# Optimization experiments

Hardware: AMD Instinct MI355X
Metric: run time of the kernel (lower is better)

The kernel has to match this reference:

```python
import jax, jax.numpy as jnp
import numpy as np

K_NEIGHBORS = 9
BN_EPS = 1e-5


def _bn(x, g, b, m, v):
    # inference-mode BatchNorm over channel (last) axis
    return (x - m) * (g / jnp.sqrt(v + BN_EPS)) + b


def _sincos_1d(dim, pos):
    half = dim // 2
    omega = 1.0 / (10000.0 ** (jnp.arange(half, dtype=jnp.float32) / half))
    ang = pos[:, None] * omega[None, :]
    return jnp.concatenate([jnp.sin(ang), jnp.cos(ang)], axis=1)


def _pos_embed_2d(dim, H, W):
    # standard 2D sin-cos positional embedding, (N, dim)
    yy, xx = jnp.meshgrid(jnp.arange(H, dtype=jnp.float32), jnp.arange(W, dtype=jnp.float32), indexing='ij')
    emb_h = _sincos_1d(dim // 2, yy.reshape(-1))
    emb_w = _sincos_1d(dim // 2, xx.reshape(-1))
    return jnp.concatenate([emb_h, emb_w], axis=1)


def setup_inputs() -> dict:
    key = jax.random.key(0)
    ks = jax.random.split(key, 8)
    B, C, H, W = 8, 192, 56, 56
    C2 = 2 * C
    Cg = C2 // 4  # per-group channels for grouped 1x1 conv
    x = jax.random.normal(ks[0], (B, C, H, W), jnp.float32)
    inp = {
        'x': x,
        'fc1_w': jax.random.normal(ks[1], (C, C), jnp.float32) * 0.05,
        'fc1_b': jnp.zeros((C,), jnp.float32),
        'bn1_g': jnp.ones((C,), jnp.float32),
        'bn1_b': jnp.zeros((C,), jnp.float32),
        'bn1_m': jax.random.normal(ks[2], (C,), jnp.float32) * 0.1,
        'bn1_v': jax.random.uniform(ks[3], (C,), jnp.float32, 0.5, 1.5),
        'gc_w': jax.random.normal(ks[4], (4, Cg, Cg), jnp.float32) * 0.05,  # groups=4, (g, out_pg, in_pg)
        'gc_b': jnp.zeros((C2,), jnp.float32),
        'bng_g': jnp.ones((C2,), jnp.float32),
        'bng_b': jnp.zeros((C2,), jnp.float32),
        'bng_m': jax.random.normal(ks[5], (C2,), jnp.float32) * 0.1,
        'bng_v': jax.random.uniform(ks[6], (C2,), jnp.float32, 0.5, 1.5),
        'fc2_w': jax.random.normal(ks[7], (C, C2), jnp.float32) * 0.05,
        'fc2_b': jnp.zeros((C,), jnp.float32),
        'bn2_g': jnp.ones((C,), jnp.float32),
        'bn2_b': jnp.zeros((C,), jnp.float32),
        'bn2_m': jnp.zeros((C,), jnp.float32),
        'bn2_v': jnp.ones((C,), jnp.float32),
    }
    return inp


def reference(x, fc1_w, fc1_b, bn1_g, bn1_b, bn1_m, bn1_v,
              gc_w, gc_b, bng_g, bng_b, bng_m, bng_v,
              fc2_w, fc2_b, bn2_g, bn2_b, bn2_m, bn2_v):
    B, C, H, W = x.shape
    N = H * W
    shortcut = x
    # fc1: 1x1 conv + BN, working in (B, N, C) layout
    h = x.reshape(B, C, N).transpose(0, 2, 1)
    h = jnp.einsum('bnc,dc->bnd', h, fc1_w) + fc1_b
    h = _bn(h, bn1_g, bn1_b, bn1_m, bn1_v)
    # relative position bias (ViG-style: -2*pe@pe.T/dim)
    pe = _pos_embed_2d(C, H, W)                      # (N, C)
    rel = (-2.0 / C) * (pe @ pe.T)                   # (N, N)
    # dense dilated kNN graph on L2-normalized features
    xn = h / jnp.maximum(jnp.linalg.norm(h, axis=-1, keepdims=True), 1e-12)
    sq = jnp.sum(xn * xn, axis=-1, keepdims=True)    # (B, N, 1)
    dist = sq - 2.0 * jnp.einsum('bnc,bmc->bnm', xn, xn) + sq.transpose(0, 2, 1)
    dist = dist + rel[None]                          # (B, N, N)
    _, nn_idx = jax.lax.top_k(-dist, K_NEIGHBORS)    # (B, N, K), dilation=1
    # MRConv2d: max-relative aggregation
    x_j = h[jnp.arange(B)[:, None, None], nn_idx]    # (B, N, K, C) gather
    d = jnp.max(x_j - h[:, :, None, :], axis=2)      # (B, N, C)
    g = jnp.concatenate([h, d], axis=-1)             # (B, N, 2C)
    # grouped 1x1 conv (groups=4) + BN + GELU
    C2 = 2 * C
    Cg = C2 // 4
    gg = g.reshape(B, N, 4, Cg)
    y = jnp.einsum('bngc,gdc->bngd', gg, gc_w).reshape(B, N, C2) + gc_b
    y = jax.nn.gelu(_bn(y, bng_g, bng_b, bng_m, bng_v), approximate=False)
    # fc2: 1x1 conv + BN, residual
    o = jnp.einsum('bnc,dc->bnd', y, fc2_w) + fc2_b
    o = _bn(o, bn2_g, bn2_b, bn2_m, bn2_v)
    out = o.transpose(0, 2, 1).reshape(B, C, H, W) + shortcut
    return out
```

## Files before the change

kernel.cpp:

```cpp
#include <hip/hip_runtime.h>
#include <math.h>

#define BATCH 8
#define CH    192
#define WW    56
#define NPTS  3136
#define C2    384
#define CG    96
#define MT    32
#define MSPLIT 4
#define LK    12
#define NCAND (MSPLIT*LK)
#define NREF  16
#define MQ    (NPTS/MSPLIT)

typedef float f32x4 __attribute__((ext_vector_type(4)));
typedef short bf16x8 __attribute__((ext_vector_type(8)));

__device__ __forceinline__ float gelu_exact(float v) {
  return 0.5f * v * (1.0f + erff(v * 0.7071067811865475f));
}
__device__ __forceinline__ unsigned short f2bf(float f) {
  unsigned int u = __float_as_uint(f);
  u = u + 0x7fffu + ((u >> 16) & 1u);
  return (unsigned short)(u >> 16);
}
__device__ __forceinline__ float bf2f(unsigned short h) {
  return __uint_as_float(((unsigned int)h) << 16);
}
__device__ __forceinline__ void gl_lds16(const void* g, void* lds) {
  __builtin_amdgcn_global_load_lds(
      (const __attribute__((address_space(1))) unsigned int*)g,
      (__attribute__((address_space(3))) unsigned int*)lds, 16, 0, 0);
}
__device__ __forceinline__ unsigned fmono(float f) {
  unsigned u = __float_as_uint(f);
  return u ^ ((unsigned)((int)u >> 31) | 0x80000000u);
}
__device__ __forceinline__ unsigned umin32(unsigned a, unsigned b) { return a < b ? a : b; }
__device__ __forceinline__ unsigned umax32(unsigned a, unsigned b) { return a < b ? b : a; }

__global__ void prep_kernel(
    const float* __restrict__ fc1_w, const float* __restrict__ fc1_b,
    const float* __restrict__ bn1_g, const float* __restrict__ bn1_b,
    const float* __restrict__ bn1_m, const float* __restrict__ bn1_v,
    const float* __restrict__ gc_w,  const float* __restrict__ gc_b,
    const float* __restrict__ bng_g, const float* __restrict__ bng_b,
    const float* __restrict__ bng_m, const float* __restrict__ bng_v,
    const float* __restrict__ fc2_w, const float* __restrict__ fc2_b,
    const float* __restrict__ bn2_g, const float* __restrict__ bn2_b,
    const float* __restrict__ bn2_m, const float* __restrict__ bn2_v,
    float* __restrict__ w1, float* __restrict__ b1,
    unsigned short* __restrict__ wgh, unsigned short* __restrict__ wgl,
    float* __restrict__ bg,
    unsigned short* __restrict__ w2h, unsigned short* __restrict__ w2l,
    float* __restrict__ b2, float* __restrict__ ftab)
{
  int i = blockIdx.x * 256 + threadIdx.x;
  if (i < 36864) {
    int d = i / CH;
    float s = bn1_g[d] / sqrtf(bn1_v[d] + 1e-5f);
    w1[i] = fc1_w[i] * s;
  } else if (i < 37056) {
    int d = i - 36864;
    float s = bn1_g[d] / sqrtf(bn1_v[d] + 1e-5f);
    b1[d] = (fc1_b[d] - bn1_m[d]) * s + bn1_b[d];
  } else if (i < 73920) {
    int j = i - 37056;
    int o = j / CG;
    float s = bng_g[o] / sqrtf(bng_v[o] + 1e-5f);
    float v = gc_w[j] * s;
    unsigned short hi = f2bf(v);
    wgh[j] = hi;
    wgl[j] = f2bf(v - bf2f(hi));
  } else if (i < 74304) {
    int o = i - 73920;
    float s = bng_g[o] / sqrtf(bng_v[o] + 1e-5f);
    bg[o] = (gc_b[o] - bng_m[o]) * s + bng_b[o];
  } else if (i < 148032) {
    int j = i - 74304;
    int d = j / C2;
    float s = bn2_g[d] / sqrtf(bn2_v[d] + 1e-5f);
    float v = fc2_w[j] * s;
    unsigned short hi = f2bf(v);
    w2h[j] = hi;
    w2l[j] = f2bf(v - bf2f(hi));
  } else if (i < 148224) {
    int d = i - 148032;
    float s = bn2_g[d] / sqrtf(bn2_v[d] + 1e-5f);
    b2[d] = (fc2_b[d] - bn2_m[d]) * s + bn2_b[d];
  } else if (i < 148280) {
    int delta = i - 148224;
    float s = 0.f;
    for (int t = 0; t < 48; ++t) {
      float omega = powf(10000.f, -(float)t / 48.f);
      s += cosf((float)delta * omega);
    }
    ftab[delta] = s * (-2.0f / (float)CH);
  }
}

__global__ __launch_bounds__(256) void fc1_kernel(
    const float* __restrict__ x, const float* __restrict__ w1,
    const float* __restrict__ b1, float* __restrict__ h)
{
  __shared__ float As[64*68];
  __shared__ float Bs[64*68];
  const int tid = threadIdx.x;
  const int ntile = blockIdx.x, dt = blockIdx.y, b = blockIdx.z;
  const int n0 = ntile * 64, d0 = dt * 64;
  const int ty = tid >> 4, tx = tid & 15;
  const float* xb = x + (size_t)b * CH * NPTS;
  float acc[4][4] = {};
  for (int k0 = 0; k0 < CH; k0 += 64) {
    if (k0) __syncthreads();
#pragma unroll
    for (int p = 0; p < 16; ++p) {
      int e = p * 256 + tid;
      int kk = e >> 6, r = e & 63;
      As[r*68 + kk] = xb[(size_t)(k0 + kk) * NPTS + n0 + r];
    }
#pragma unroll
    for (int p = 0; p < 4; ++p) {
      int e = p * 256 + tid;
      int dd = e >> 4, k4 = (e & 15) << 2;
      *(float4*)&Bs[dd*68 + k4] = *(const float4*)&w1[(size_t)(d0 + dd) * CH + k0 + k4];
    }
    __syncthreads();
#pragma unroll
    for (int kq = 0; kq < 16; ++kq) {
      float4 av[4], bv[4];
#pragma unroll
      for (int i = 0; i < 4; ++i) av[i] = *(const float4*)&As[(ty*4+i)*68 + kq*4];
#pragma unroll
      for (int j = 0; j < 4; ++j) bv[j] = *(const float4*)&Bs[(tx*4+j)*68 + kq*4];
#pragma unroll
      for (int i = 0; i < 4; ++i)
#pragma unroll
        for (int j = 0; j < 4; ++j)
          acc[i][j] += av[i].x*bv[j].x + av[i].y*bv[j].y + av[i].z*bv[j].z + av[i].w*bv[j].w;
    }
  }
#pragma unroll
  for (int i = 0; i < 4; ++i) {
    int n = n0 + ty*4 + i;
    float4 v;
    v.x = acc[i][0] + b1[d0 + tx*4 + 0];
    v.y = acc[i][1] + b1[d0 + tx*4 + 1];
    v.z = acc[i][2] + b1[d0 + tx*4 + 2];
    v.w = acc[i][3] + b1[d0 + tx*4 + 3];
    *(float4*)&h[((size_t)b * NPTS + n) * CH + d0 + tx*4] = v;
  }
}

__global__ __launch_bounds__(256) void norm_kernel(
    const float* __restrict__ h, float* __restrict__ xnf,
    unsigned short* __restrict__ xhi, unsigned short* __restrict__ xlo,
    float* __restrict__ sqv)
{
  const int lane = threadIdx.x & 63;
  const int row = blockIdx.x * 4 + (threadIdx.x >> 6);
  const float* hr = h + (size_t)row * CH;
  float v0 = hr[lane], v1 = hr[lane + 64], v2 = hr[lane + 128];
  float s = v0*v0 + v1*v1 + v2*v2;
#pragma unroll
  for (int o = 32; o > 0; o >>= 1) s += __shfl_xor(s, o);
  float inv = 1.0f / fmaxf(sqrtf(s), 1e-12f);
  float x0 = v0 * inv, x1 = v1 * inv, x2 = v2 * inv;
  size_t base = (size_t)row * CH;
  xnf[base + lane      ] = x0;
  xnf[base + lane + 64 ] = x1;
  xnf[base + lane + 128] = x2;
  unsigned short h0 = f2bf(x0), h1 = f2bf(x1), h2 = f2bf(x2);
  xhi[base + lane      ] = h0;
  xhi[base + lane + 64 ] = h1;
  xhi[base + lane + 128] = h2;
  xlo[base + lane      ] = f2bf(x0 - bf2f(h0));
  xlo[base + lane + 64 ] = f2bf(x1 - bf2f(h1));
  xlo[base + lane + 128] = f2bf(x2 - bf2f(h2));
  if (lane == 0) sqv[row] = s * inv * inv;
}

__global__ __launch_bounds__(256, 3) void topk_kernel(
    const unsigned short* __restrict__ xhi, const unsigned short* __restrict__ xlo,
    const float* __restrict__ fts_g,
    unsigned* __restrict__ pd)
{
  __shared__ __align__(16) char LDSbuf[2 * 24576];
  __shared__ float ft[64];

  const int tid  = threadIdx.x;
  const int lane = tid & 63;
  const int w    = tid >> 6;
  const int bid  = blockIdx.x;
  const int b    = bid & 7;
  const int r_   = bid >> 3;
  const int ms   = r_ / 49;
  const int nt   = r_ % 49;
  const int n0 = nt * 64;
  const size_t rowbase = (size_t)b * NPTS;

  if (tid < 64) ft[tid] = (tid < 56) ? fts_g[tid] : 0.0f;

  const int ar = lane & 15;
  const int hi = lane >> 4;
  const int ak = hi * 8;

  const int n_b = n0 + w * 16 + ar;
  bf16x8 bhi[6], blo[6];
  {
    const unsigned short* pbh = xhi + (rowbase + n_b) * CH + ak;
    const unsigned short* pbl = xlo + (rowbase + n_b) * CH + ak;
#pragma unroll
    for (int c = 0; c < 6; ++c) {
      bhi[c] = *(const bf16x8*)(pbh + c * 32);
      blo[c] = *(const bf16x8*)(pbl + c * 32);
    }
  }
  const int yn_l = n_b / WW, xn_l = n_b % WW;

  unsigned ld[LK];
#pragma unroll
  for (int k = 0; k < LK; ++k) ld[k] = 0xFFFFFFFFu;

  int srcb[6];
#pragma unroll
  for (int j = 0; j < 6; ++j) {
    int L = (w & 1) * 6144 + j * 1024 + lane * 16;
    int r = L / 384, off = L % 384;
    srcb[j] = r * 384 + (off ^ ((r & 7) << 4));
  }
  const int ldsb = (w >= 2 ? 12288 : 0) + (w & 1) * 6144;

  const int mbase = ms * MQ;
  const char* gb = (w < 2 ? (const char*)xhi : (const char*)xlo)
                   + (rowbase + mbase) * (CH * 2);

#define STAGE(BUF) do {                                                     \
  _Pragma("unroll")                                                         \
  for (int j = 0; j < 6; ++j)                                               \
    gl_lds16(gb + srcb[j], LDSbuf + (BUF) * 24576 + ldsb + j * 1024);       \
} while (0)

  STAGE(0);
  gb += 12288;

  int ym0 = ms * 14, xm0 = 0;

  for (int tt = 0; tt < 25; ++tt) {
    __syncthreads();
    if (tt + 1 < 25) { STAGE((tt + 1) & 1); gb += 12288; }

    const int bufb = (tt & 1) * 24576;
    const int swz = (ar & 7) << 4;
    const float fdy0 = ft[abs(yn_l - ym0)];
    const float fdy1 = ft[abs(yn_l - ym0 - 1)];
    const int nrt = (tt == 24) ? 1 : 2;
#pragma unroll
    for (int rt = 0; rt < 2; ++rt) {
      if (rt >= nrt) break;
      const int rA = rt * 16 + ar;
      f32x4 a_hh = {}, a_hl = {}, a_lh = {};
#pragma unroll
      for (int c = 0; c < 6; ++c) {
        int off = bufb + rA * 384 + ((c * 64 + hi * 16) ^ swz);
        bf16x8 ah = *(const bf16x8*)(LDSbuf + off);
        bf16x8 al = *(const bf16x8*)(LDSbuf + off + 12288);
        a_hh = __builtin_amdgcn_mfma_f32_16x16x32_bf16(ah, bhi[c], a_hh, 0, 0, 0);
        a_hl = __builtin_amdgcn_mfma_f32_16x16x32_bf16(ah, blo[c], a_hl, 0, 0, 0);
        a_lh = __builtin_amdgcn_mfma_f32_16x16x32_bf16(al, bhi[c], a_lh, 0, 0, 0);
      }
      f32x4 s4;
#pragma unroll
      for (int i = 0; i < 4; ++i) s4[i] = a_hh[i] + (a_hl[i] + a_lh[i]);

      const int locb = tt * MT + rt * 16 + hi * 4;
      unsigned kk[4];
#pragma unroll
      for (int i = 0; i < 4; ++i) {
        int xm = xm0 + rt * 16 + hi * 4 + i;
        const bool wrap = (xm >= WW);
        if (wrap) xm -= WW;
        int dx = xn_l - xm; dx = dx < 0 ? -dx : dx;
        float d_ = (wrap ? fdy1 : fdy0) + ft[dx] - 2.0f * s4[i];
        kk[i] = (fmono(d_) & 0xFFFFFC00u) | (unsigned)(locb + i);
      }
      {
        unsigned sa = umax32(kk[0], kk[1]), sb = umin32(kk[0], kk[1]);
        unsigned sc = umax32(kk[2], kk[3]), sd = umin32(kk[2], kk[3]);
        unsigned v0 = umax32(sa, sc), t1 = umin32(sa, sc);
        unsigned t2 = umax32(sb, sd), v3 = umin32(sb, sd);
        unsigned v1 = umax32(t1, t2), v2 = umin32(t1, t2);
        unsigned l4 = umin32(ld[4], v0), g4 = umax32(ld[4], v0);
        unsigned l5 = umin32(ld[5], v1), g5 = umax32(ld[5], v1);
        unsigned l6 = umin32(ld[6], v2), g6 = umax32(ld[6], v2);
        unsigned l7 = umin32(ld[7], v3), g7 = umax32(ld[7], v3);
        unsigned a0 = umin32(ld[0], l4), b0 = umax32(ld[0], l4);
        unsigned a1 = umin32(ld[1], l5), b1 = umax32(ld[1], l5);
        unsigned a2 = umin32(ld[2], l6), b2 = umax32(ld[2], l6);
        unsigned a3 = umin32(ld[3], l7), b3 = umax32(ld[3], l7);
        unsigned q0 = umin32(a0, a2), q2 = umax32(a0, a2);
        unsigned q1 = umin32(a1, a3), q3 = umax32(a1, a3);
        unsigned r0 = umin32(b0, b2), r2 = umax32(b0, b2);
        unsigned r1 = umin32(b1, b3), r3 = umax32(b1, b3);
        ld[0] = umin32(q0, q1); ld[1] = umax32(q0, q1);
        ld[2] = umin32(q2, q3); ld[3] = umax32(q2, q3);
        ld[4] = umin32(r0, r1); ld[5] = umax32(r0, r1);
        ld[6] = umin32(r2, r3); ld[7] = umax32(r2, r3);
        unsigned e0 = umin32(ld[8],  g4);
        unsigned e1 = umin32(ld[9],  g5);
        unsigned e2 = umin32(ld[10], g6);
        unsigned e3 = umin32(ld[11], g7);
        unsigned f0 = umin32(e0, e2), f2 = umax32(e0, e2);
        unsigned f1 = umin32(e1, e3), f3 = umax32(e1, e3);
        ld[8]  = umin32(f0, f1); ld[9]  = umax32(f0, f1);
        ld[10] = umin32(f2, f3); ld[11] = umax32(f2, f3);
      }
    }
    xm0 += MT;
    if (xm0 >= WW) { xm0 -= WW; ym0 += 1; }
  }

  __syncthreads();
  unsigned* Md = (unsigned*)LDSbuf;
#pragma unroll
  for (int k = 0; k < LK; ++k) Md[tid * LK + k] = ld[k];
  __syncthreads();
  if (tid < 64) {
    const int wv = tid >> 4, arr = tid & 15;
    const int n = n0 + tid;
    int lb[4];
#pragma unroll
    for (int hq = 0; hq < 4; ++hq) lb[hq] = (wv * 64 + hq * 16 + arr) * LK;
    int p0 = 0, p1 = 0, p2 = 0, p3 = 0;
    unsigned* od = pd + ((rowbase + n) * MSPLIT + ms) * LK;
    for (int k = 0; k < LK; ++k) {
      unsigned bk = Md[lb[0] + p0]; int bq = 0;
      unsigned v1 = Md[lb[1] + p1];
      if (v1 < bk) { bk = v1; bq = 1; }
      unsigned v2 = Md[lb[2] + p2];
      if (v2 < bk) { bk = v2; bq = 2; }
      unsigned v3 = Md[lb[3] + p3];
      if (v3 < bk) { bk = v3; bq = 3; }
      if (bq == 0) { if (p0 < LK-1) ++p0; else Md[lb[0]+p0] = 0xFFFFFFFFu; }
      else if (bq == 1) { if (p1 < LK-1) ++p1; else Md[lb[1]+p1] = 0xFFFFFFFFu; }
      else if (bq == 2) { if (p2 < LK-1) ++p2; else Md[lb[2]+p2] = 0xFFFFFFFFu; }
      else              { if (p3 < LK-1) ++p3; else Md[lb[3]+p3] = 0xFFFFFFFFu; }
      od[k] = bk;
    }
  }
#undef STAGE
}

__global__ __launch_bounds__(256) void refine_kernel(
    const unsigned* __restrict__ pd,
    const float* __restrict__ xn, const float* __restrict__ sqv,
    const float* __restrict__ fts_g, int* __restrict__ nn)
{
  __shared__ unsigned allk[4][NCAND];
  __shared__ int      ci_s[4][NREF];
  __shared__ float ft[56];
  const int tid = threadIdx.x;
  const int w = tid >> 6, lane = tid & 63;
  if (tid < 56) ft[tid] = fts_g[tid];
  const int row = blockIdx.x * 4 + w;
  const int b = row / NPTS;
  const int n_loc = row - b * NPTS;

  if (lane < NCAND) allk[w][lane] = pd[(size_t)row * NCAND + lane];
  __syncthreads();
  if (lane < NCAND) {
    unsigned k0 = allk[w][lane];
    int rank = 0;
    for (int j = 0; j < NCAND; ++j) {
      unsigned kj = allk[w][j];
      rank += (kj < k0 || (kj == k0 && j < lane)) ? 1 : 0;
    }
    if (rank < NREF) ci_s[w][rank] = (lane / LK) * MQ + (int)(k0 & 1023u);
  }
  __syncthreads();

  const float* xrow = xn + (size_t)row * CH;
  float a0 = xrow[lane], a1 = xrow[lane + 64], a2 = xrow[lane + 128];
  const int yn_ = n_loc / WW, xq_ = n_loc % WW;
  const size_t xbase = (size_t)b * NPTS * CH;

  int cm[NREF];
  float xv0[NREF], xv1[NREF], xv2[NREF];
#pragma unroll
  for (int c = 0; c < NREF; ++c) {
    int m = ci_s[w][c];
    cm[c] = m;
    const float* xm = xn + xbase + (size_t)m * CH;
    xv0[c] = xm[lane];
    xv1[c] = xm[lane + 64];
    xv2[c] = xm[lane + 128];
  }

  float myd = INFINITY; int myi = 0x7fffffff;
#pragma unroll
  for (int c = 0; c < NREF; ++c) {
    float s = a0 * xv0[c] + a1 * xv1[c] + a2 * xv2[c];
#pragma unroll
    for (int o = 32; o > 0; o >>= 1) s += __shfl_xor(s, o);
    if (lane == c) {
      int m = cm[c];
      int ym = m / WW, xm_ = m % WW;
      int dy = yn_ - ym; dy = dy < 0 ? -dy : dy;
      int dx = xq_ - xm_; dx = dx < 0 ? -dx : dx;
      myd = sqv[(size_t)b * NPTS + m] - 2.0f * s + (ft[dy] + ft[dx]);
      myi = m;
    }
  }
  if (lane < NREF) {
    int rank = 0;
    for (int j = 0; j < NREF; ++j) {
      float dj = __shfl(myd, j); int ij = __shfl(myi, j);
      rank += (dj < myd || (dj == myd && ij < myi)) ? 1 : 0;
    }
    if (rank < 9) nn[(size_t)row * 9 + rank] = myi;
  }
}

__global__ __launch_bounds__(256, 4) void gc_kernel(
    const float* __restrict__ h, const int* __restrict__ nn,
    const unsigned short* __restrict__ wgh, const unsigned short* __restrict__ wgl,
    const float* __restrict__ bg, unsigned short* __restrict__ y)
{
  __shared__ __align__(16) char Wb[2 * 18432];
  __shared__ int nns[576];
  const int tid = threadIdx.x;
  const int lane = tid & 63;
  const int w = tid >> 6;
  const int rt = blockIdx.x, g = blockIdx.y;
  const int n0g = rt * 64;
  const int b = n0g / NPTS;
  const size_t rowbase = (size_t)b * NPTS;
  const int cb = (g & 1) * CG;
  const int cn = lane & 15;
  const int kq = lane >> 4;
  const bool isD = (g >= 2);

  {
    const char* gh = (const char*)wgh + (size_t)g * 96 * 192;
    const char* gl = (const char*)wgl + (size_t)g * 96 * 192;
    for (int c = tid; c < 1152; c += 256) {
      int L = c * 16;
      int row = L / 192;
      int slot = (L % 192) >> 4;
      int sb = row * 192 + ((slot ^ (row & 3)) << 4);
      gl_lds16(gh + sb, Wb + L);
      gl_lds16(gl + sb, Wb + 18432 + L);
    }
  }
  if (isD) {
    for (int e = tid; e < 576; e += 256)
      nns[e] = nn[(size_t)(n0g + e / 9) * 9 + (e % 9)];
  }
  __syncthreads();

  const int rloc = w * 16 + cn;
  const int nb = n0g + rloc;
  bf16x8 gh8[3], gl8[3];
#pragma unroll
  for (int c = 0; c < 3; ++c) {
    const float* base = h + (size_t)nb * CH + cb + c * 32 + kq * 8;
    float4 x0 = *(const float4*)base;
    float4 x1 = *(const float4*)(base + 4);
    if (isD) {
      float4 m0 = make_float4(-INFINITY, -INFINITY, -INFINITY, -INFINITY);
      float4 m1 = m0;
#pragma unroll
      for (int k = 0; k < 9; ++k) {
        const float* nbase = h + (rowbase + nns[rloc * 9 + k]) * CH + cb + c * 32 + kq * 8;
        float4 n0v = *(const float4*)nbase;
        float4 n1v = *(const float4*)(nbase + 4);
        m0.x = fmaxf(m0.x, n0v.x); m0.y = fmaxf(m0.y, n0v.y);
        m0.z = fmaxf(m0.z, n0v.z); m0.w = fmaxf(m0.w, n0v.w);
        m1.x = fmaxf(m1.x, n1v.x); m1.y = fmaxf(m1.y, n1v.y);
        m1.z = fmaxf(m1.z, n1v.z); m1.w = fmaxf(m1.w, n1v.w);
      }
      x0.x = m0.x - x0.x; x0.y = m0.y - x0.y; x0.z = m0.z - x0.z; x0.w = m0.w - x0.w;
      x1.x = m1.x - x1.x; x1.y = m1.y - x1.y; x1.z = m1.z - x1.z; x1.w = m1.w - x1.w;
    }
    float v[8];
    *(float4*)&v[0] = x0;
    *(float4*)&v[4] = x1;
#pragma unroll
    for (int j = 0; j < 8; ++j) {
      unsigned short hh = f2bf(v[j]);
      gh8[c][j] = (short)hh;
      gl8[c][j] = (short)f2bf(v[j] - bf2f(hh));
    }
  }

#pragma unroll
  for (int sub = 0; sub < 6; ++sub) {
    f32x4 acc = {};
#pragma unroll
    for (int c = 0; c < 3; ++c) {
      int row = sub * 16 + cn;
      int slot = c * 4 + kq;
      int off = row * 192 + ((slot ^ (row & 3)) << 4);
      bf16x8 ah = *(const bf16x8*)(Wb + off);
      bf16x8 al = *(const bf16x8*)(Wb + 18432 + off);
      acc = __builtin_amdgcn_mfma_f32_16x16x32_bf16(ah, gh8[c], acc, 0, 0, 0);
      acc = __builtin_amdgcn_mfma_f32_16x16x32_bf16(ah, gl8[c], acc, 0, 0, 0);
      acc = __builtin_amdgcn_mfma_f32_16x16x32_bf16(al, gh8[c], acc, 0, 0, 0);
    }
    const int ocb = g * CG + sub * 16 + kq * 4;
    unsigned short pk[4];
#pragma unroll
    for (int i = 0; i < 4; ++i)
      pk[i] = f2bf(gelu_exact(acc[i] + bg[ocb + i]));
    *(ushort4*)&y[(size_t)nb * C2 + ocb] = *(ushort4*)pk;
  }
}

__global__ __launch_bounds__(256, 4) void fc2_kernel(
    const unsigned short* __restrict__ yv,
    const unsigned short* __restrict__ w2h, const unsigned short* __restrict__ w2l,
    const float* __restrict__ b2, const float* __restrict__ x, float* __restrict__ out)
{
  __shared__ __align__(16) char Wb[2 * 12288];
  const int tid = threadIdx.x;
  const int lane = tid & 63;
  const int w = tid >> 6;
  const int rt = blockIdx.x, dg = blockIdx.y;
  const int n0g = rt * 64;
  const int b = n0g / NPTS;
  const int nloc0 = n0g - b * NPTS;
  const int cn = lane & 15;
  const int kk0 = (lane >> 4) * 8;

  bf16x8 yb[12];
  {
    const unsigned short* yp = yv + (size_t)(n0g + w * 16 + cn) * C2 + kk0;
#pragma unroll
    for (int c = 0; c < 12; ++c) yb[c] = *(const bf16x8*)(yp + c * 32);
  }

  int srcb[3], dstb[3];
#pragma unroll
  for (int j = 0; j < 3; ++j) {
    int L = (w * 3 + j) * 1024 + lane * 16;
    int r = L / 768, off = L % 768;
    srcb[j] = r * 768 + (off ^ ((r & 7) << 4));
    dstb[j] = (w * 3 + j) * 1024;
  }

  const char* gh = (const char*)w2h + (size_t)dg * 64 * 768;
  const char* gl = (const char*)w2l + (size_t)dg * 64 * 768;
  const int rr = cn;
  const int swz = (rr & 7) << 4;
  const int nsp = nloc0 + w * 16 + cn;

  for (int ds = 0; ds < 4; ++ds) {
    __syncthreads();
#pragma unroll
    for (int j = 0; j < 3; ++j) {
      gl_lds16(gh + ds * 12288 + srcb[j], Wb + dstb[j]);
      gl_lds16(gl + ds * 12288 + srcb[j], Wb + 12288 + dstb[j]);
    }
    __syncthreads();

    f32x4 acc_h = {}, acc_l = {};
#pragma unroll
    for (int c = 0; c < 12; ++c) {
      int off = rr * 768 + ((c * 64 + (lane >> 4) * 16) ^ swz);
      bf16x8 ah = *(const bf16x8*)(Wb + off);
      bf16x8 al = *(const bf16x8*)(Wb + 12288 + off);
      acc_h = __builtin_amdgcn_mfma_f32_16x16x32_bf16(ah, yb[c], acc_h, 0, 0, 0);
      acc_l = __builtin_amdgcn_mfma_f32_16x16x32_bf16(al, yb[c], acc_l, 0, 0, 0);
    }
    const int d0 = dg * 64 + ds * 16;
#pragma unroll
    for (int i = 0; i < 4; ++i) {
      int d = d0 + (lane >> 4) * 4 + i;
      size_t gi = ((size_t)b * CH + d) * NPTS + nsp;
      out[gi] = acc_h[i] + acc_l[i] + b2[d] + x[gi];
    }
  }
}

extern "C" void kernel_launch(void* const* d_in, const int* in_sizes, int n_in,
                              void* d_out, int out_size, void* d_ws, size_t ws_size,
                              hipStream_t stream) {
  const float* x     = (const float*)d_in[0];
  const float* fc1_w = (const float*)d_in[1];
  const float* fc1_b = (const float*)d_in[2];
  const float* bn1_g = (const float*)d_in[3];
  const float* bn1_b = (const float*)d_in[4];
  const float* bn1_m = (const float*)d_in[5];
  const float* bn1_v = (const float*)d_in[6];
  const float* gc_w  = (const float*)d_in[7];
  const float* gc_b  = (const float*)d_in[8];
  const float* bng_g = (const float*)d_in[9];
  const float* bng_b = (const float*)d_in[10];
  const float* bng_m = (const float*)d_in[11];
  const float* bng_v = (const float*)d_in[12];
  const float* fc2_w = (const float*)d_in[13];
  const float* fc2_b = (const float*)d_in[14];
  const float* bn2_g = (const float*)d_in[15];
  const float* bn2_b = (const float*)d_in[16];
  const float* bn2_m = (const float*)d_in[17];
  const float* bn2_v = (const float*)d_in[18];

  float* ws = (float*)d_ws;
  size_t o = 0;
  float* W1 = ws + o; o += 36864;
  float* B1 = ws + o; o += 192;
  unsigned short* WGH = (unsigned short*)(ws + o); o += 18432;
  unsigned short* WGL = (unsigned short*)(ws + o); o += 18432;
  float* BG = ws + o; o += 384;
  unsigned short* W2H = (unsigned short*)(ws + o); o += 36864;
  unsigned short* W2L = (unsigned short*)(ws + o); o += 36864;
  float* B2 = ws + o; o += 192;
  float* FT = ws + o; o += 64;
  float* H  = ws + o; o += (size_t)25088 * 192;
  float* SQ = ws + o; o += 25088;
  int*   NN = (int*)(ws + o); o += 25088 * 9;
  float* SCR = ws + o;
  unsigned short* XHI = (unsigned short*)SCR;
  unsigned short* XLO = XHI + (size_t)4816896;
  float* XN  = SCR + (size_t)4816896;
  unsigned short* YB = (unsigned short*)XN;
  unsigned* PD = (unsigned*)(XN + (size_t)4816896);
  (void)ws_size; (void)in_sizes; (void)n_in; (void)out_size;

  hipLaunchKernelGGL(prep_kernel, dim3(580), dim3(256), 0, stream,
                     fc1_w, fc1_b, bn1_g, bn1_b, bn1_m, bn1_v,
                     gc_w, gc_b, bng_g, bng_b, bng_m, bng_v,
                     fc2_w, fc2_b, bn2_g, bn2_b, bn2_m, bn2_v,
                     W1, B1, WGH, WGL, BG, W2H, W2L, B2, FT);
  hipLaunchKernelGGL(fc1_kernel, dim3(49, 3, 8), dim3(256), 0, stream, x, W1, B1, H);
  hipLaunchKernelGGL(norm_kernel, dim3(6272), dim3(256), 0, stream, H, XN, XHI, XLO, SQ);
  hipLaunchKernelGGL(topk_kernel, dim3(49 * MSPLIT * 8), dim3(256), 0, stream, XHI, XLO, FT, PD);
  hipLaunchKernelGGL(refine_kernel, dim3(6272), dim3(256), 0, stream, PD, XN, SQ, FT, NN);
  hipLaunchKernelGGL(gc_kernel, dim3(392, 4), dim3(256), 0, stream, H, NN, WGH, WGL, BG, YB);
  hipLaunchKernelGGL(fc2_kernel, dim3(392, 3), dim3(256), 0, stream, YB, W2H, W2L, B2, x, (float*)d_out);
}
```

Before: 364.0 us.

## Pre-transpose x and double-buffer fc1 tiles with async global-to-LDS loads

Adds a separate transpose kernel that writes x into a point-major layout. fc1 can then stream contiguous 16-byte rows straight into LDS through gl_lds16 into an XOR-swizzled, double-buffered shared tile, so the next K tile loads while the current one is computed. This removes the strided scalar loads of x in fc1 and the bank conflicts of the old padded layout. In exchange it adds one extra kernel launch and a full read and write of x (about 19 MB) through a scratch buffer, and the larger LDS footprint may limit occupancy.

Result: slower. 429.4 us (+17.9%).

```diff
diff --git a/kernel.cpp b/kernel.cpp
--- a/kernel.cpp
+++ b/kernel.cpp
@@ -100,40 +100,85 @@
   }
 }
 
-__global__ __launch_bounds__(256) void fc1_kernel(
-    const float* __restrict__ x, const float* __restrict__ w1,
+__global__ __launch_bounds__(256) void xt_kernel(
+    const float* __restrict__ x, float* __restrict__ xt)
+{
+  __shared__ float T[64 * 65];
+  const int tid = threadIdx.x;
+  const int nt = blockIdx.x, kt = blockIdx.y, b = blockIdx.z;
+  const int n0 = nt * 64, k0 = kt * 64;
+  const float* xb = x + (size_t)b * CH * NPTS;
+#pragma unroll
+  for (int p = 0; p < 16; ++p) {
+    int e = p * 256 + tid;
+    int kk = e >> 6, r = e & 63;
+    T[kk * 65 + r] = xb[(size_t)(k0 + kk) * NPTS + n0 + r];
+  }
+  __syncthreads();
+#pragma unroll
+  for (int p = 0; p < 4; ++p) {
+    int e = p * 256 + tid;
+    int r = e >> 4, k4 = (e & 15) << 2;
+    float4 v;
+    v.x = T[(k4 + 0) * 65 + r];
+    v.y = T[(k4 + 1) * 65 + r];
+    v.z = T[(k4 + 2) * 65 + r];
+    v.w = T[(k4 + 3) * 65 + r];
+    *(float4*)&xt[((size_t)b * NPTS + n0 + r) * CH + k0 + k4] = v;
+  }
+}
+
+__global__ __launch_bounds__(256, 2) void fc1_kernel(
+    const float* __restrict__ xt, const float* __restrict__ w1,
     const float* __restrict__ b1, float* __restrict__ h)
 {
-  __shared__ float As[64*68];
-  __shared__ float Bs[64*68];
+  __shared__ __align__(16) char FB[2 * 32768];
   const int tid = threadIdx.x;
   const int ntile = blockIdx.x, dt = blockIdx.y, b = blockIdx.z;
   const int n0 = ntile * 64, d0 = dt * 64;
   const int ty = tid >> 4, tx = tid & 15;
-  const float* xb = x + (size_t)b * CH * NPTS;
+
+  int srow[4], soff[4], dstl[4];
+#pragma unroll
+  for (int j = 0; j < 4; ++j) {
+    int c = tid + 256 * j;
+    srow[j] = c >> 4;
+    soff[j] = (((c & 15) ^ (srow[j] & 7)) << 4);
+    dstl[j] = c * 16;
+  }
+  const char* xa = (const char*)(xt + ((size_t)b * NPTS + n0) * CH);
+  const char* wb = (const char*)(w1 + (size_t)d0 * CH);
+
+#define FSTAGE(BUF, KT) do {                                                   \
+  _Pragma("unroll")                                                            \
+  for (int j = 0; j < 4; ++j) {                                                \
+    gl_lds16(xa + (size_t)srow[j] * 768 + (KT) * 256 + soff[j],                \
+             FB + (BUF) * 32768 + dstl[j]);                                    \
+    gl_lds16(wb + (size_t)srow[j] * 768 + (KT) * 256 + soff[j],                \
+             FB + (BUF) * 32768 + 16384 + dstl[j]);                            \
+  }                                                                            \
+} while (0)
+
   float acc[4][4] = {};
-  for (int k0 = 0; k0 < CH; k0 += 64) {
-    if (k0) __syncthreads();
-#pragma unroll
-    for (int p = 0; p < 16; ++p) {
-      int e = p * 256 + tid;
-      int kk = e >> 6, r = e & 63;
-      As[r*68 + kk] = xb[(size_t)(k0 + kk) * NPTS + n0 + r];
-    }
-#pragma unroll
-    for (int p = 0; p < 4; ++p) {
-      int e = p * 256 + tid;
-      int dd = e >> 4, k4 = (e & 15) << 2;
-      *(float4*)&Bs[dd*68 + k4] = *(const float4*)&w1[(size_t)(d0 + dd) * CH + k0 + k4];
-    }
+  FSTAGE(0, 0);
+  for (int kt = 0; kt < 3; ++kt) {
     __syncthreads();
+    if (kt < 2) FSTAGE((kt + 1) & 1, kt + 1);
+    const char* As = FB + (kt & 1) * 32768;
+    const char* Bs = As + 16384;
 #pragma unroll
     for (int kq = 0; kq < 16; ++kq) {
       float4 av[4], bv[4];
 #pragma unroll
-      for (int i = 0; i < 4; ++i) av[i] = *(const float4*)&As[(ty*4+i)*68 + kq*4];
-#pragma unroll
-      for (int j = 0; j < 4; ++j) bv[j] = *(const float4*)&Bs[(tx*4+j)*68 + kq*4];
+      for (int i = 0; i < 4; ++i) {
+        int r = ty * 4 + i;
+        av[i] = *(const float4*)(As + r * 256 + ((kq << 4) ^ ((r & 7) << 4)));
+      }
+#pragma unroll
+      for (int j = 0; j < 4; ++j) {
+        int r = tx * 4 + j;
+        bv[j] = *(const float4*)(Bs + r * 256 + ((kq << 4) ^ ((r & 7) << 4)));
+      }
 #pragma unroll
       for (int i = 0; i < 4; ++i)
 #pragma unroll
@@ -141,6 +186,7 @@
           acc[i][j] += av[i].x*bv[j].x + av[i].y*bv[j].y + av[i].z*bv[j].z + av[i].w*bv[j].w;
     }
   }
+#undef FSTAGE
 #pragma unroll
   for (int i = 0; i < 4; ++i) {
     int n = n0 + ty*4 + i;
@@ -621,6 +667,7 @@
   float* SQ = ws + o; o += 25088;
   int*   NN = (int*)(ws + o); o += 25088 * 9;
   float* SCR = ws + o;
+  float* XT  = SCR;
   unsigned short* XHI = (unsigned short*)SCR;
   unsigned short* XLO = XHI + (size_t)4816896;
   float* XN  = SCR + (size_t)4816896;
@@ -633,7 +680,8 @@
                      gc_w, gc_b, bng_g, bng_b, bng_m, bng_v,
                      fc2_w, fc2_b, bn2_g, bn2_b, bn2_m, bn2_v,
                      W1, B1, WGH, WGL, BG, W2H, W2L, B2, FT);
-  hipLaunchKernelGGL(fc1_kernel, dim3(49, 3, 8), dim3(256), 0, stream, x, W1, B1, H);
+  hipLaunchKernelGGL(xt_kernel, dim3(49, 3, 8), dim3(256), 0, stream, x, XT);
+  hipLaunchKernelGGL(fc1_kernel, dim3(49, 3, 8), dim3(256), 0, stream, XT, W1, B1, H);
   hipLaunchKernelGGL(norm_kernel, dim3(6272), dim3(256), 0, stream, H, XN, XHI, XLO, SQ);
   hipLaunchKernelGGL(topk_kernel, dim3(49 * MSPLIT * 8), dim3(256), 0, stream, XHI, XLO, FT, PD);
   hipLaunchKernelGGL(refine_kernel, dim3(6272), dim3(256), 0, stream, PD, XN, SQ, FT, NN);
```

## Pre-transpose input to point-major layout and XOR-swizzle fc1 shared tiles

Applied to the files above, without the earlier changes.

Adds a transpose kernel that writes x as (B, N, C) into scratch, so fc1 can load its activation tile with float4 row reads instead of scattered scalar stores into shared memory. fc1's shared tiles now use an XOR swizzle on the column index to avoid bank conflicts on the vectorised reads. In exchange there is an extra kernel launch plus a full extra read and write of the input tensor, and fc1 is a small part of the total pipeline.

After: 361.1 us, median of 2. No clear change (-0.8%).

```diff
diff --git a/kernel.cpp b/kernel.cpp
--- a/kernel.cpp
+++ b/kernel.cpp
@@ -100,8 +100,36 @@
   }
 }
 
+__global__ __launch_bounds__(256) void xt_kernel(
+    const float* __restrict__ x, float* __restrict__ xt)
+{
+  __shared__ float T[64 * 65];
+  const int tid = threadIdx.x;
+  const int nt = blockIdx.x, kt = blockIdx.y, b = blockIdx.z;
+  const int n0 = nt * 64, k0 = kt * 64;
+  const float* xb = x + (size_t)b * CH * NPTS;
+#pragma unroll
+  for (int p = 0; p < 16; ++p) {
+    int e = p * 256 + tid;
+    int kk = e >> 6, r = e & 63;
+    T[kk * 65 + r] = xb[(size_t)(k0 + kk) * NPTS + n0 + r];
+  }
+  __syncthreads();
+#pragma unroll
+  for (int p = 0; p < 4; ++p) {
+    int e = p * 256 + tid;
+    int r = e >> 4, k4 = (e & 15) << 2;
+    float4 v;
+    v.x = T[(k4 + 0) * 65 + r];
+    v.y = T[(k4 + 1) * 65 + r];
+    v.z = T[(k4 + 2) * 65 + r];
+    v.w = T[(k4 + 3) * 65 + r];
+    *(float4*)&xt[((size_t)b * NPTS + n0 + r) * CH + k0 + k4] = v;
+  }
+}
+
 __global__ __launch_bounds__(256) void fc1_kernel(
-    const float* __restrict__ x, const float* __restrict__ w1,
+    const float* __restrict__ xt, const float* __restrict__ w1,
     const float* __restrict__ b1, float* __restrict__ h)
 {
   __shared__ float As[64*68];
@@ -110,30 +138,30 @@
   const int ntile = blockIdx.x, dt = blockIdx.y, b = blockIdx.z;
   const int n0 = ntile * 64, d0 = dt * 64;
   const int ty = tid >> 4, tx = tid & 15;
-  const float* xb = x + (size_t)b * CH * NPTS;
+  const float* xa = xt + ((size_t)b * NPTS + n0) * CH;
+  const float* wb = w1 + (size_t)d0 * CH;
+  const int tya = ty & 7, txa = tx & 7;
   float acc[4][4] = {};
   for (int k0 = 0; k0 < CH; k0 += 64) {
     if (k0) __syncthreads();
 #pragma unroll
-    for (int p = 0; p < 16; ++p) {
-      int e = p * 256 + tid;
-      int kk = e >> 6, r = e & 63;
-      As[r*68 + kk] = xb[(size_t)(k0 + kk) * NPTS + n0 + r];
-    }
-#pragma unroll
     for (int p = 0; p < 4; ++p) {
       int e = p * 256 + tid;
-      int dd = e >> 4, k4 = (e & 15) << 2;
-      *(float4*)&Bs[dd*68 + k4] = *(const float4*)&w1[(size_t)(d0 + dd) * CH + k0 + k4];
+      int r = e >> 4, c4 = e & 15;
+      int col = (c4 ^ ((r >> 2) & 7)) << 2;
+      *(float4*)&As[r*68 + col] = *(const float4*)&xa[(size_t)r * CH + k0 + (c4 << 2)];
+      *(float4*)&Bs[r*68 + col] = *(const float4*)&wb[(size_t)r * CH + k0 + (c4 << 2)];
     }
     __syncthreads();
 #pragma unroll
     for (int kq = 0; kq < 16; ++kq) {
+      const int ca = (kq ^ tya) << 2;
+      const int cb = (kq ^ txa) << 2;
       float4 av[4], bv[4];
 #pragma unroll
-      for (int i = 0; i < 4; ++i) av[i] = *(const float4*)&As[(ty*4+i)*68 + kq*4];
-#pragma unroll
-      for (int j = 0; j < 4; ++j) bv[j] = *(const float4*)&Bs[(tx*4+j)*68 + kq*4];
+      for (int i = 0; i < 4; ++i) av[i] = *(const float4*)&As[(ty*4+i)*68 + ca];
+#pragma unroll
+      for (int j = 0; j < 4; ++j) bv[j] = *(const float4*)&Bs[(tx*4+j)*68 + cb];
 #pragma unroll
       for (int i = 0; i < 4; ++i)
 #pragma unroll
@@ -621,6 +649,7 @@
   float* SQ = ws + o; o += 25088;
   int*   NN = (int*)(ws + o); o += 25088 * 9;
   float* SCR = ws + o;
+  float* XT  = SCR;
   unsigned short* XHI = (unsigned short*)SCR;
   unsigned short* XLO = XHI + (size_t)4816896;
   float* XN  = SCR + (size_t)4816896;
@@ -633,7 +662,8 @@
                      gc_w, gc_b, bng_g, bng_b, bng_m, bng_v,
                      fc2_w, fc2_b, bn2_g, bn2_b, bn2_m, bn2_v,
                      W1, B1, WGH, WGL, BG, W2H, W2L, B2, FT);
-  hipLaunchKernelGGL(fc1_kernel, dim3(49, 3, 8), dim3(256), 0, stream, x, W1, B1, H);
+  hipLaunchKernelGGL(xt_kernel, dim3(49, 3, 8), dim3(256), 0, stream, x, XT);
+  hipLaunchKernelGGL(fc1_kernel, dim3(49, 3, 8), dim3(256), 0, stream, XT, W1, B1, H);
   hipLaunchKernelGGL(norm_kernel, dim3(6272), dim3(256), 0, stream, H, XN, XHI, XLO, SQ);
   hipLaunchKernelGGL(topk_kernel, dim3(49 * MSPLIT * 8), dim3(256), 0, stream, XHI, XLO, FT, PD);
   hipLaunchKernelGGL(refine_kernel, dim3(6272), dim3(256), 0, stream, PD, XN, SQ, FT, NN);
```
